# Performance work log

Measured on AMD Instinct MI355X. Metric: run time of the kernel, lower is better.

Reference implementation:

```python
import jax, jax.numpy as jnp
import numpy as np

THRESHOLD = 1e-3  # hardcoded `thresholds = 0.001` in the sparse branch


def setup_inputs() -> dict:
    key = jax.random.key(0)
    k1, k2, k3, k4, k5 = jax.random.split(key, 5)
    b, r, d_in, d_out = 8, 4096, 768, 768
    x = jax.random.normal(k1, (b, r, d_in), dtype=jnp.float32)
    weight = jax.random.normal(k2, (d_out, d_in), dtype=jnp.float32) * 0.02
    bias = jax.random.normal(k3, (d_out,), dtype=jnp.float32) * 0.02
    U = jax.random.normal(k4, (d_in, d_in), dtype=jnp.float32) * (d_in ** -0.5)
    VT = jax.random.normal(k5, (d_out, d_out), dtype=jnp.float32) * (d_out ** -0.5)
    return {"x": x, "weight": weight, "bias": bias, "U": U, "VT": VT}


def reference(x, weight, bias, U, VT):
    # Sparse path (len_grads >= 30) of LinearFunctionSparseGrad.forward.
    # h = x @ U.T, rotated into the gradient basis.  [b, r, c]
    h = jnp.einsum('brc,dc->brd', x, U)
    # Threshold-sparsify: zero entries with |h| <= 0.001.
    h = jnp.where(jnp.abs(h) > THRESHOLD, h, jnp.zeros((), h.dtype))
    # Original: gather nonzero rows/cols, h[rows][:, cols] @ weight.T[cols],
    # then scatter back via I[:, rows] @ res_. Dropped cols are exactly-zero
    # columns and dropped rows are exactly-zero rows, so the math equals a
    # dense matmul on the masked tensor (no [b*r, b*r] identity needed).
    res = jnp.einsum('brc,oc->bro', h, weight)        # h @ weight.T
    res = jnp.einsum('bro,po->brp', res, VT)          # res_ @ VT.T (self.VT=VT_orig.T => VT here)
    return res + bias
```

## Files before the change

kernel.cpp:

```cpp
#include <hip/hip_runtime.h>
#include <hip/hip_bf16.h>

typedef __bf16 bf16_t;
typedef bf16_t bf16x8 __attribute__((ext_vector_type(8)));
typedef bf16_t bf16x4 __attribute__((ext_vector_type(4)));
typedef float  f32x4  __attribute__((ext_vector_type(4)));

#define BM 128
#define BN 128
#define BK 32

enum { EPI_NONE = 0, EPI_THRESH = 1, EPI_BIAS = 2 };

template <int EPI, typename CT>
__global__ __launch_bounds__(256, 2)
void gemm_bt(const bf16_t* __restrict__ A, const bf16_t* __restrict__ B,
             CT* __restrict__ C, const float* __restrict__ bias,
             int M, int N, int K)
{
    __shared__ __align__(16) bf16_t As[BM][BK];
    __shared__ __align__(16) bf16_t Bs[BN][BK];

    const int lane = threadIdx.x & 63;
    const int wave = threadIdx.x >> 6;
    const int wm = wave >> 1;
    const int wn = wave & 1;
    const int m0 = blockIdx.y * BM;
    const int n0 = blockIdx.x * BN;

    const int ar = lane >> 2;
    const int ac = (lane & 3) * 8;

    const int fm   = lane & 15;
    const int kq   = (lane >> 4) * 8;
    const int quad = lane >> 4;

    f32x4 acc[4][4];
#pragma unroll
    for (int i = 0; i < 4; i++)
#pragma unroll
        for (int j = 0; j < 4; j++) acc[i][j] = {0.f, 0.f, 0.f, 0.f};

    for (int k0 = 0; k0 < K; k0 += BK) {
#pragma unroll
        for (int i = 0; i < 2; i++) {
            const int chunk = wave * 2 + i;
            const bf16_t* ga = A + (size_t)(m0 + chunk * 16 + ar) * K + k0 + ac;
            __builtin_amdgcn_global_load_lds(
                (const __attribute__((address_space(1))) void*)ga,
                (__attribute__((address_space(3))) void*)&As[chunk * 16][0],
                16, 0, 0);
            const bf16_t* gb = B + (size_t)(n0 + chunk * 16 + ar) * K + k0 + ac;
            __builtin_amdgcn_global_load_lds(
                (const __attribute__((address_space(1))) void*)gb,
                (__attribute__((address_space(3))) void*)&Bs[chunk * 16][0],
                16, 0, 0);
        }
        __syncthreads();

        bf16x8 af[4], bfr[4];
#pragma unroll
        for (int i = 0; i < 4; i++)
            af[i] = *(const bf16x8*)&As[wm * 64 + i * 16 + fm][kq];
#pragma unroll
        for (int j = 0; j < 4; j++)
            bfr[j] = *(const bf16x8*)&Bs[wn * 64 + j * 16 + fm][kq];

#pragma unroll
        for (int i = 0; i < 4; i++)
#pragma unroll
            for (int j = 0; j < 4; j++)
                acc[i][j] = __builtin_amdgcn_mfma_f32_16x16x32_bf16(
                    af[i], bfr[j], acc[i][j], 0, 0, 0);

        __syncthreads();
    }

#pragma unroll
    for (int i = 0; i < 4; i++) {
#pragma unroll
        for (int j = 0; j < 4; j++) {
            const int col = n0 + wn * 64 + j * 16 + fm;
            float bv = 0.f;
            if (EPI == EPI_BIAS) bv = bias[col];
#pragma unroll
            for (int r = 0; r < 4; r++) {
                const int row = m0 + wm * 64 + i * 16 + quad * 4 + r;
                float v = acc[i][j][r];
                if (EPI == EPI_THRESH) v = (fabsf(v) > 1e-3f) ? v : 0.f;
                if (EPI == EPI_BIAS) v += bv;
                C[(size_t)row * N + col] = (CT)v;
            }
        }
    }
}

__global__ void cvt_f32_bf16(const float* __restrict__ in,
                             bf16_t* __restrict__ out, int n4)
{
    const int i = blockIdx.x * blockDim.x + threadIdx.x;
    if (i < n4) {
        const f32x4 v = ((const f32x4*)in)[i];
        bf16x4 o;
        o[0] = (bf16_t)v[0]; o[1] = (bf16_t)v[1];
        o[2] = (bf16_t)v[2]; o[3] = (bf16_t)v[3];
        ((bf16x4*)out)[i] = o;
    }
}

__global__ void transpose_cvt(const float* __restrict__ in,
                              bf16_t* __restrict__ out, int n)
{
    __shared__ float t[32][33];
    const int bx = blockIdx.x * 32, by = blockIdx.y * 32;
    const int tx = threadIdx.x, ty = threadIdx.y;
#pragma unroll
    for (int i = 0; i < 32; i += 8)
        t[ty + i][tx] = in[(size_t)(by + ty + i) * n + bx + tx];
    __syncthreads();
#pragma unroll
    for (int i = 0; i < 32; i += 8)
        out[(size_t)(bx + ty + i) * n + by + tx] = (bf16_t)t[tx][ty + i];
}

extern "C" void kernel_launch(void* const* d_in, const int* in_sizes, int n_in,
                              void* d_out, int out_size, void* d_ws, size_t ws_size,
                              hipStream_t stream)
{
    const float* x    = (const float*)d_in[0];
    const float* w    = (const float*)d_in[1];
    const float* bias = (const float*)d_in[2];
    const float* U    = (const float*)d_in[3];
    const float* VT   = (const float*)d_in[4];
    float* out = (float*)d_out;

    const int D = 768;
    const int M = 8 * 4096;
    const size_t MD = (size_t)M * D;
    const size_t DD = (size_t)D * D;

    char* ws = (char*)d_ws;
    bf16_t* xb  = (bf16_t*)ws;
    bf16_t* h   = (bf16_t*)(ws + MD * 2);
    bf16_t* Ub  = (bf16_t*)(ws + MD * 4);
    bf16_t* VTb = (bf16_t*)(ws + MD * 4 + DD * 2);
    bf16_t* Wt  = (bf16_t*)(ws + MD * 4 + DD * 4);
    bf16_t* Wc  = (bf16_t*)(ws + MD * 4 + DD * 6);

    cvt_f32_bf16<<<(int)(MD / 4 / 256), 256, 0, stream>>>(x, xb, (int)(MD / 4));
    cvt_f32_bf16<<<(int)(DD / 4 / 256), 256, 0, stream>>>(U, Ub, (int)(DD / 4));
    cvt_f32_bf16<<<(int)(DD / 4 / 256), 256, 0, stream>>>(VT, VTb, (int)(DD / 4));
    transpose_cvt<<<dim3(D / 32, D / 32), dim3(32, 8), 0, stream>>>(w, Wt, D);

    gemm_bt<EPI_NONE, bf16_t><<<dim3(D / BN, D / BM), 256, 0, stream>>>(
        VTb, Wt, Wc, nullptr, D, D, D);
    gemm_bt<EPI_THRESH, bf16_t><<<dim3(D / BN, M / BM), 256, 0, stream>>>(
        xb, Ub, h, nullptr, M, D, D);
    gemm_bt<EPI_BIAS, float><<<dim3(D / BN, M / BM), 256, 0, stream>>>(
        h, Wc, out, bias, M, D, D);
}
```

Measured before the change: 334.6 us.

## Fuse prep kernels, co-launch weight GEMM with h GEMM, widen BK with swizzled LDS

Merges the four conversion and transpose kernels into a single prep launch, and runs the small VT·W weight-combine GEMM inside the same grid as the large x·U GEMM. This cuts seven launches to three. The GEMM K-tile is doubled to 64, which halves the number of barriers per tile, and the LDS layout now uses an XOR swizzle to avoid bank conflicts on fragment reads. The price is twice the LDS per block, which may lower occupancy, and the fused kernel carries a divergent branch between tile types.

Result: faster. 313.0 us (-6.4%).

```diff
diff --git a/kernel.cpp b/kernel.cpp
--- a/kernel.cpp
+++ b/kernel.cpp
@@ -8,32 +8,29 @@
 
 #define BM 128
 #define BN 128
-#define BK 32
+#define BK 64
 
 enum { EPI_NONE = 0, EPI_THRESH = 1, EPI_BIAS = 2 };
 
+
 template <int EPI, typename CT>
-__global__ __launch_bounds__(256, 2)
-void gemm_bt(const bf16_t* __restrict__ A, const bf16_t* __restrict__ B,
-             CT* __restrict__ C, const float* __restrict__ bias,
-             int M, int N, int K)
+__device__ __forceinline__
+void gemm_tile(const bf16_t* __restrict__ A, const bf16_t* __restrict__ B,
+               CT* __restrict__ C, const float* __restrict__ bias,
+               int m0, int n0, int N, int K,
+               bf16_t* As, bf16_t* Bs)
 {
-    __shared__ __align__(16) bf16_t As[BM][BK];
-    __shared__ __align__(16) bf16_t Bs[BN][BK];
-
     const int lane = threadIdx.x & 63;
     const int wave = threadIdx.x >> 6;
     const int wm = wave >> 1;
     const int wn = wave & 1;
-    const int m0 = blockIdx.y * BM;
-    const int n0 = blockIdx.x * BN;
 
-    const int ar = lane >> 2;
-    const int ac = (lane & 3) * 8;
+    const int srow = lane >> 3;
+    const int scg  = (lane & 7) ^ ((lane >> 3) & 7);
 
-    const int fm   = lane & 15;
-    const int kq   = (lane >> 4) * 8;
-    const int quad = lane >> 4;
+    const int fm = lane & 15;
+    const int q  = lane >> 4;
+    const int fsw = fm & 7;
 
     f32x4 acc[4][4];
 #pragma unroll
@@ -43,36 +40,42 @@
 
     for (int k0 = 0; k0 < K; k0 += BK) {
 #pragma unroll
-        for (int i = 0; i < 2; i++) {
-            const int chunk = wave * 2 + i;
-            const bf16_t* ga = A + (size_t)(m0 + chunk * 16 + ar) * K + k0 + ac;
+        for (int i = 0; i < 4; i++) {
+            const int ubase = wave * 256 + i * 64;
+            const int row   = (ubase >> 3) + srow;
+            const bf16_t* ga = A + (size_t)(m0 + row) * K + k0 + scg * 8;
             __builtin_amdgcn_global_load_lds(
                 (const __attribute__((address_space(1))) void*)ga,
-                (__attribute__((address_space(3))) void*)&As[chunk * 16][0],
+                (__attribute__((address_space(3))) void*)(As + (size_t)ubase * 8),
                 16, 0, 0);
-            const bf16_t* gb = B + (size_t)(n0 + chunk * 16 + ar) * K + k0 + ac;
+            const bf16_t* gb = B + (size_t)(n0 + row) * K + k0 + scg * 8;
             __builtin_amdgcn_global_load_lds(
                 (const __attribute__((address_space(1))) void*)gb,
-                (__attribute__((address_space(3))) void*)&Bs[chunk * 16][0],
+                (__attribute__((address_space(3))) void*)(Bs + (size_t)ubase * 8),
                 16, 0, 0);
         }
         __syncthreads();
 
-        bf16x8 af[4], bfr[4];
 #pragma unroll
-        for (int i = 0; i < 4; i++)
-            af[i] = *(const bf16x8*)&As[wm * 64 + i * 16 + fm][kq];
+        for (int h = 0; h < 2; h++) {
+            bf16x8 af[4], bfr[4];
 #pragma unroll
-        for (int j = 0; j < 4; j++)
-            bfr[j] = *(const bf16x8*)&Bs[wn * 64 + j * 16 + fm][kq];
-
+            for (int i = 0; i < 4; i++) {
+                const int row = wm * 64 + i * 16 + fm;
+                af[i] = *(const bf16x8*)(As + (size_t)(row * 8 + ((h * 4 + q) ^ fsw)) * 8);
+            }
 #pragma unroll
-        for (int i = 0; i < 4; i++)
+            for (int j = 0; j < 4; j++) {
+                const int row = wn * 64 + j * 16 + fm;
+                bfr[j] = *(const bf16x8*)(Bs + (size_t)(row * 8 + ((h * 4 + q) ^ fsw)) * 8);
+            }
 #pragma unroll
-            for (int j = 0; j < 4; j++)
-                acc[i][j] = __builtin_amdgcn_mfma_f32_16x16x32_bf16(
-                    af[i], bfr[j], acc[i][j], 0, 0, 0);
-
+            for (int i = 0; i < 4; i++)
+#pragma unroll
+                for (int j = 0; j < 4; j++)
+                    acc[i][j] = __builtin_amdgcn_mfma_f32_16x16x32_bf16(
+                        af[i], bfr[j], acc[i][j], 0, 0, 0);
+        }
         __syncthreads();
     }
 
@@ -85,7 +88,7 @@
             if (EPI == EPI_BIAS) bv = bias[col];
 #pragma unroll
             for (int r = 0; r < 4; r++) {
-                const int row = m0 + wm * 64 + i * 16 + quad * 4 + r;
+                const int row = m0 + wm * 64 + i * 16 + q * 4 + r;
                 float v = acc[i][j][r];
                 if (EPI == EPI_THRESH) v = (fabsf(v) > 1e-3f) ? v : 0.f;
                 if (EPI == EPI_BIAS) v += bv;
@@ -95,32 +98,66 @@
     }
 }
 
-__global__ void cvt_f32_bf16(const float* __restrict__ in,
-                             bf16_t* __restrict__ out, int n4)
+__global__ __launch_bounds__(256)
+void gemm_h_wc(const bf16_t* __restrict__ xb, const bf16_t* __restrict__ Ub,
+               bf16_t* __restrict__ h,
+               const bf16_t* __restrict__ VTb, const bf16_t* __restrict__ Wt,
+               bf16_t* __restrict__ Wc)
 {
-    const int i = blockIdx.x * blockDim.x + threadIdx.x;
-    if (i < n4) {
-        const f32x4 v = ((const f32x4*)in)[i];
+    __shared__ __align__(16) bf16_t As[BM * BK];
+    __shared__ __align__(16) bf16_t Bs[BN * BK];
+    const int b = blockIdx.x;
+    if (b < 1536) {
+        gemm_tile<EPI_THRESH, bf16_t>(xb, Ub, h, nullptr,
+                                      (b / 6) * BM, (b % 6) * BN, 768, 768, As, Bs);
+    } else {
+        const int b2 = b - 1536;
+        gemm_tile<EPI_NONE, bf16_t>(VTb, Wt, Wc, nullptr,
+                                    (b2 / 6) * BM, (b2 % 6) * BN, 768, 768, As, Bs);
+    }
+}
+
+__global__ __launch_bounds__(256)
+void gemm_out(const bf16_t* __restrict__ h, const bf16_t* __restrict__ Wc,
+              float* __restrict__ out, const float* __restrict__ bias)
+{
+    __shared__ __align__(16) bf16_t As[BM * BK];
+    __shared__ __align__(16) bf16_t Bs[BN * BK];
+    const int b = blockIdx.x;
+    gemm_tile<EPI_BIAS, float>(h, Wc, out, bias,
+                               (b / 6) * BM, (b % 6) * BN, 768, 768, As, Bs);
+}
+
+__global__ __launch_bounds__(256)
+void prep(const float* __restrict__ x, const float* __restrict__ U,
+          const float* __restrict__ VT, const float* __restrict__ w,
+          bf16_t* __restrict__ xb, bf16_t* __restrict__ Ub,
+          bf16_t* __restrict__ VTb, bf16_t* __restrict__ Wt)
+{
+    __shared__ float tt[32][33];
+    const int b = blockIdx.x;
+    if (b < 25728) {
+        const float* src; bf16_t* dst; int i;
+        if (b < 24576)      { src = x;  dst = xb;  i = b * 256 + threadIdx.x; }
+        else if (b < 25152) { src = U;  dst = Ub;  i = (b - 24576) * 256 + threadIdx.x; }
+        else                { src = VT; dst = VTb; i = (b - 25152) * 256 + threadIdx.x; }
+        const f32x4 v = ((const f32x4*)src)[i];
         bf16x4 o;
         o[0] = (bf16_t)v[0]; o[1] = (bf16_t)v[1];
         o[2] = (bf16_t)v[2]; o[3] = (bf16_t)v[3];
-        ((bf16x4*)out)[i] = o;
+        ((bf16x4*)dst)[i] = o;
+    } else {
+        const int t = b - 25728;
+        const int bx = (t % 24) * 32, by = (t / 24) * 32;
+        const int tx = threadIdx.x & 31, ty = threadIdx.x >> 5;
+#pragma unroll
+        for (int i = 0; i < 32; i += 8)
+            tt[ty + i][tx] = w[(size_t)(by + ty + i) * 768 + bx + tx];
+        __syncthreads();
+#pragma unroll
+        for (int i = 0; i < 32; i += 8)
+            Wt[(size_t)(bx + ty + i) * 768 + by + tx] = (bf16_t)tt[tx][ty + i];
     }
-}
-
-__global__ void transpose_cvt(const float* __restrict__ in,
-                              bf16_t* __restrict__ out, int n)
-{
-    __shared__ float t[32][33];
-    const int bx = blockIdx.x * 32, by = blockIdx.y * 32;
-    const int tx = threadIdx.x, ty = threadIdx.y;
-#pragma unroll
-    for (int i = 0; i < 32; i += 8)
-        t[ty + i][tx] = in[(size_t)(by + ty + i) * n + bx + tx];
-    __syncthreads();
-#pragma unroll
-    for (int i = 0; i < 32; i += 8)
-        out[(size_t)(bx + ty + i) * n + by + tx] = (bf16_t)t[tx][ty + i];
 }
 
 extern "C" void kernel_launch(void* const* d_in, const int* in_sizes, int n_in,
@@ -147,15 +184,7 @@
     bf16_t* Wt  = (bf16_t*)(ws + MD * 4 + DD * 4);
     bf16_t* Wc  = (bf16_t*)(ws + MD * 4 + DD * 6);
 
-    cvt_f32_bf16<<<(int)(MD / 4 / 256), 256, 0, stream>>>(x, xb, (int)(MD / 4));
-    cvt_f32_bf16<<<(int)(DD / 4 / 256), 256, 0, stream>>>(U, Ub, (int)(DD / 4));
-    cvt_f32_bf16<<<(int)(DD / 4 / 256), 256, 0, stream>>>(VT, VTb, (int)(DD / 4));
-    transpose_cvt<<<dim3(D / 32, D / 32), dim3(32, 8), 0, stream>>>(w, Wt, D);
-
-    gemm_bt<EPI_NONE, bf16_t><<<dim3(D / BN, D / BM), 256, 0, stream>>>(
-        VTb, Wt, Wc, nullptr, D, D, D);
-    gemm_bt<EPI_THRESH, bf16_t><<<dim3(D / BN, M / BM), 256, 0, stream>>>(
-        xb, Ub, h, nullptr, M, D, D);
-    gemm_bt<EPI_BIAS, float><<<dim3(D / BN, M / BM), 256, 0, stream>>>(
-        h, Wc, out, bias, M, D, D);
+    prep<<<26304, 256, 0, stream>>>(x, U, VT, w, xb, Ub, VTb, Wt);
+    gemm_h_wc<<<1536 + 36, 256, 0, stream>>>(xb, Ub, h, VTb, Wt, Wc);
+    gemm_out<<<1536, 256, 0, stream>>>(h, Wc, out, bias);
 }
```
